# Optimization experiments

Measured on AMD Instinct MI355X. Metric: run time of the kernel, lower is better.

Reference implementation:

```python
import jax, jax.numpy as jnp
import numpy as np

B, T, D, H = 4, 2048, 1024, 16
HD = D // H  # head_dim = 64
SCALE = HD ** -0.5


def setup_inputs() -> dict:
    key = jax.random.key(0)
    k1, k2, k3 = jax.random.split(key, 3)
    x = jax.random.normal(k1, (B, T, D), dtype=jnp.float32)
    # xavier-uniform-like scaling for weights
    qkv_w = jax.random.normal(k2, (3 * D, D), dtype=jnp.float32) * (2.0 / (4 * D)) ** 0.5
    out_w = jax.random.normal(k3, (D, D), dtype=jnp.float32) * (1.0 / D) ** 0.5
    out_b = jnp.zeros((D,), dtype=jnp.float32)
    return {"x": x, "qkv_w": qkv_w, "out_w": out_w, "out_b": out_b}


def reference(x, qkv_w, out_w, out_b):
    Bx, Tx, _ = x.shape
    # qkv projection (nn.Linear: x @ W^T), no bias
    qkv = jnp.einsum('btd,ed->bte', x, qkv_w)  # [B,T,3D]
    qkv = qkv.reshape(Bx, Tx, 3, H, HD).transpose(2, 0, 3, 1, 4)  # [3,B,H,T,hd]
    q, k, v = qkv[0], qkv[1], qkv[2]
    scores = jnp.einsum('bhqd,bhkd->bhqk', q, k) * SCALE  # [B,H,T,T]
    causal = jnp.triu(jnp.ones((Tx, Tx), dtype=bool), k=1)
    scores = jnp.where(causal, -jnp.inf, scores)
    weights = jax.nn.softmax(scores, axis=-1)
    out = jnp.einsum('bhqk,bhkd->bhqd', weights, v)  # [B,H,T,hd]
    out = out.transpose(0, 2, 1, 3).reshape(Bx, Tx, D)
    return jnp.einsum('btd,ed->bte', out, out_w) + out_b
```

## Files before the change

kernel.cpp:

```cpp
#include <hip/hip_runtime.h>
#include <stdint.h>


typedef __bf16 bfx8 __attribute__((ext_vector_type(8)));
typedef float f32x4 __attribute__((ext_vector_type(4)));
typedef float f32x16 __attribute__((ext_vector_type(16)));

__device__ __forceinline__ uint16_t f2b(float f) {
  uint32_t u = __float_as_uint(f);
  u += 0x7fff + ((u >> 16) & 1);
  return (uint16_t)(u >> 16);
}

__device__ __forceinline__ uint32_t cvt_pk(float lo, float hi) {
  uint32_t r;
  asm("v_cvt_pk_bf16_f32 %0, %1, %2" : "=v"(r) : "v"(lo), "v"(hi));
  return r;
}

__device__ __forceinline__ void gld16(const void* g, void* l) {
  __builtin_amdgcn_global_load_lds((const __attribute__((address_space(1))) void*)g,
                                   (__attribute__((address_space(3))) void*)l,
                                   16, 0, 0);
}

__global__ __launch_bounds__(256) void cvt_all(const float* __restrict__ x,
                                               const float* __restrict__ w1,
                                               const float* __restrict__ w2,
                                               uint16_t* __restrict__ xb,
                                               uint16_t* __restrict__ w1b,
                                               uint16_t* __restrict__ w2b) {
  int i = blockIdx.x * 256 + threadIdx.x;
  const float* in;
  uint16_t* out;
  if (i < 1048576) { in = x; out = xb; }
  else if (i < 1048576 + 393216) { in = w1; out = w1b; i -= 1048576; }
  else { in = w2; out = w2b; i -= 1048576 + 393216; }
  float4 a = ((const float4*)in)[2 * i];
  float4 b = ((const float4*)in)[2 * i + 1];
  union { uint16_t u[8]; uint4 v; } pk;
  pk.u[0] = f2b(a.x); pk.u[1] = f2b(a.y); pk.u[2] = f2b(a.z); pk.u[3] = f2b(a.w);
  pk.u[4] = f2b(b.x); pk.u[5] = f2b(b.y); pk.u[6] = f2b(b.z); pk.u[7] = f2b(b.w);
  ((uint4*)out)[i] = pk.v;
}

template <int OUTF32>
__global__ __launch_bounds__(256) void gemm_bt(const uint16_t* __restrict__ A,
                                               const uint16_t* __restrict__ B,
                                               void* __restrict__ Cout,
                                               const float* __restrict__ bias,
                                               int M, int N, int K, int nbx, int nwg) {
  __shared__ alignas(16) uint16_t As[2][128 * 32];
  __shared__ alignas(16) uint16_t Bs[2][128 * 32];

  int did = blockIdx.x;
  int wg = (did & 7) * (nwg >> 3) + (did >> 3);
  int bx = wg % nbx, by = wg / nbx;
  int m0 = by * 128, n0 = bx * 128;

  int tid = threadIdx.x;
  int lane = tid & 63, wid = tid >> 6;
  int wm = wid >> 1, wn = wid & 1;

  int rs = wid * 16 + (lane >> 2);
  int cs = (lane & 3) * 8;

  f32x4 acc[4][4] = {};

  auto stage = [&](int buf, int kt) {
    int k0 = kt * 32;
    gld16(&A[(size_t)(m0 + rs) * K + k0 + cs],      &As[buf][wid * 512]);
    gld16(&A[(size_t)(m0 + rs + 64) * K + k0 + cs], &As[buf][wid * 512 + 2048]);
    gld16(&B[(size_t)(n0 + rs) * K + k0 + cs],      &Bs[buf][wid * 512]);
    gld16(&B[(size_t)(n0 + rs + 64) * K + k0 + cs], &Bs[buf][wid * 512 + 2048]);
  };

  stage(0, 0);
  __syncthreads();

  int nk = K >> 5;
  int cur = 0;
  int ko = (lane >> 4) * 8;
  for (int kt = 0; kt < nk; ++kt) {
    if (kt + 1 < nk) stage(cur ^ 1, kt + 1);
    bfx8 a[4], b[4];
#pragma unroll
    for (int mi = 0; mi < 4; ++mi)
      a[mi] = *(const bfx8*)&As[cur][(wm * 64 + mi * 16 + (lane & 15)) * 32 + ko];
#pragma unroll
    for (int ni = 0; ni < 4; ++ni)
      b[ni] = *(const bfx8*)&Bs[cur][(wn * 64 + ni * 16 + (lane & 15)) * 32 + ko];
#pragma unroll
    for (int mi = 0; mi < 4; ++mi)
#pragma unroll
      for (int ni = 0; ni < 4; ++ni)
        acc[mi][ni] =
            __builtin_amdgcn_mfma_f32_16x16x32_bf16(a[mi], b[ni], acc[mi][ni], 0, 0, 0);
    __syncthreads();
    cur ^= 1;
  }

#pragma unroll
  for (int mi = 0; mi < 4; ++mi) {
    int row = m0 + wm * 64 + mi * 16 + ((lane >> 4) << 2);
#pragma unroll
    for (int ni = 0; ni < 4; ++ni) {
      int col = n0 + wn * 64 + ni * 16 + (lane & 15);
#pragma unroll
      for (int r = 0; r < 4; ++r) {
        float v = acc[mi][ni][r];
        if (OUTF32)
          ((float*)Cout)[(size_t)(row + r) * N + col] = v + bias[col];
        else
          ((uint16_t*)Cout)[(size_t)(row + r) * N + col] = f2b(v);
      }
    }
  }
}

__global__ __launch_bounds__(256, 2) void flash_attn(const uint16_t* __restrict__ qkv,
                                                     uint16_t* __restrict__ attnb) {
  const int T = 2048, D3 = 3072;
  const float CSC = 0.125f * 1.44269504f;
  __shared__ alignas(16) uint16_t Ks[3][64 * 64];
  __shared__ alignas(16) uint16_t Vt[3][64 * 64];

  int did = blockIdx.x;
  int c = did & 255;
  int j = did >> 8;
  int bh = c >> 2, tr = c & 3;
  int b = bh >> 4, h = bh & 15;

  int tid = threadIdx.x, lane = tid & 63, wid = tid >> 6;
  int l31 = lane & 31, hi = lane >> 5;
  int swz = (lane & 7) << 3;

  size_t base = (size_t)b * T * D3;
  int hoff = h * 64;
  const uint16_t* kbase = &qkv[base + 1024 + hoff];
  const uint16_t* vbase = &qkv[base + 2048 + hoff];

  int krow = wid * 16 + (lane >> 3);
  int kc = ((lane & 7) << 3) ^ ((krow & 7) << 3);
  int vr = (tid & 31) * 2;
  int vc = (tid >> 5) * 8;

  int nparts = (j == 2) ? 2 : 1;
  for (int p = 0; p < nparts; ++p) {
    int qb = (j == 0) ? (15 - tr) : (j == 1) ? (8 + tr) : ((p == 0) ? (7 - tr) : tr);
    int q0 = qb << 7;
    int qw = q0 + wid * 32;
    int ntile = 2 * qb + 2;

    float mC = -1e30f, l_r = 0.f;
    f32x16 acc0 = {}, acc1 = {};
    bfx8 pf[4];
    int smax_prev = -1, vb_prev = 0;

    bfx8 qf[4];
    {
      const uint16_t* qp = &qkv[base + (size_t)(qw + l31) * D3 + hoff + 8 * hi];
#pragma unroll
      for (int h4 = 0; h4 < 4; ++h4) qf[h4] = *(const bfx8*)(qp + 16 * h4);
    }

    uint4 vA0, vA1, vB0, vB1;

    auto loadV = [&](int kv0, uint4& r0, uint4& r1) {
      r0 = *(const uint4*)&vbase[(size_t)(kv0 + vr) * D3 + vc];
      r1 = *(const uint4*)&vbase[(size_t)(kv0 + vr + 1) * D3 + vc];
    };
    auto stageK = [&](int buf, int kv0) {
      gld16(&kbase[(size_t)(kv0 + krow) * D3 + kc], &Ks[buf][wid * 1024]);
      gld16(&kbase[(size_t)(kv0 + krow + 8) * D3 + kc], &Ks[buf][wid * 1024 + 512]);
    };
    auto writeV = [&](int vb, const uint4& r0, const uint4& r1) {
      union { uint4 v; uint16_t u[8]; } x, y;
      x.v = r0; y.v = r1;
#pragma unroll
      for (int jj = 0; jj < 8; ++jj) {
        int hd = vc + jj;
        uint32_t pk = (uint32_t)x.u[jj] | ((uint32_t)y.u[jj] << 16);
        *(uint32_t*)&Vt[vb][hd * 64 + (vr ^ ((hd & 7) << 3))] = pk;
      }
    };
    auto doPV = [&]() {
      const uint16_t* vp = &Vt[vb_prev][0];
      __builtin_amdgcn_s_setprio(1);
#pragma unroll
      for (int s = 0; s < 4; ++s) {
        if (s <= smax_prev) {
          bfx8 v0 = *(const bfx8*)&vp[l31 * 64 + ((16 * s + 8 * hi) ^ swz)];
          acc0 = __builtin_amdgcn_mfma_f32_32x32x16_bf16(v0, pf[s], acc0, 0, 0, 0);
          bfx8 v1 = *(const bfx8*)&vp[(32 + l31) * 64 + ((16 * s + 8 * hi) ^ swz)];
          acc1 = __builtin_amdgcn_mfma_f32_32x32x16_bf16(v1, pf[s], acc1, 0, 0, 0);
        }
      }
      __builtin_amdgcn_s_setprio(0);
    };

    loadV(0, vA0, vA1);
    stageK(0, 0);
    writeV(0, vA0, vA1);
    loadV(64, vB0, vB1);
    stageK(1, 64);
    asm volatile("s_waitcnt vmcnt(0) lgkmcnt(0)" ::: "memory");
    __builtin_amdgcn_s_barrier();
    __builtin_amdgcn_sched_barrier(0);

    auto subiter = [&](int t, uint4& f0, uint4& f1, uint4& c0, uint4& c1) {
      int kv0 = t << 6;
      bool issue = (t + 2 < ntile);
      if (issue) {
        loadV((t + 2) << 6, f0, f1);
        stageK((t + 2) % 3, (t + 2) << 6);
      }
      bool active = (kv0 <= qw);
      int tmax = (qw > kv0) ? 2 : 1;
      f32x16 st0 = {}, st1 = {};
      if (active) {
        const uint16_t* kp = &Ks[t % 3][0];
        __builtin_amdgcn_s_setprio(1);
#pragma unroll
        for (int h4 = 0; h4 < 4; ++h4) {
          bfx8 kf0 = *(const bfx8*)&kp[l31 * 64 + ((16 * h4 + 8 * hi) ^ swz)];
          st0 = __builtin_amdgcn_mfma_f32_32x32x16_bf16(kf0, qf[h4], st0, 0, 0, 0);
          if (tmax == 2) {
            bfx8 kf1 = *(const bfx8*)&kp[(32 + l31) * 64 + ((16 * h4 + 8 * hi) ^ swz)];
            st1 = __builtin_amdgcn_mfma_f32_32x32x16_bf16(kf1, qf[h4], st1, 0, 0, 0);
          }
        }
        __builtin_amdgcn_s_setprio(0);
      }

      if (smax_prev >= 0) { doPV(); smax_prev = -1; }

      if (active) {
        int q = qw + l31;
        float mx0 = -1e30f, mx1 = -1e30f;
        if (kv0 == qw) {
#pragma unroll
          for (int r = 0; r < 16; ++r) {
            int kv = kv0 + (r & 3) + 8 * (r >> 2) + 4 * hi;
            float v = st0[r];
            if (kv > q) v = -1e30f;
            st0[r] = v;
            mx0 = fmaxf(mx0, v);
          }
        } else {
#pragma unroll
          for (int r = 0; r < 16; ++r) mx0 = fmaxf(mx0, st0[r]);
        }
        if (tmax == 2) {
          if (kv0 + 32 == qw) {
#pragma unroll
            for (int r = 0; r < 16; ++r) {
              int kv = kv0 + 32 + (r & 3) + 8 * (r >> 2) + 4 * hi;
              float v = st1[r];
              if (kv > q) v = -1e30f;
              st1[r] = v;
              mx1 = fmaxf(mx1, v);
            }
          } else {
#pragma unroll
            for (int r = 0; r < 16; ++r) mx1 = fmaxf(mx1, st1[r]);
          }
        }
        float mS = fmaxf(mx0, mx1) * CSC;
        if (!__all(mS - mC <= 8.0f)) {
          float mSp = fmaxf(mS, __shfl_xor(mS, 32));
          float mCn = fmaxf(mC, mSp);
          float fac = __builtin_amdgcn_exp2f(mC - mCn);
          mC = mCn;
          l_r *= fac;
          acc0 *= fac;
          acc1 *= fac;
        }
        float l0 = 0.f, l1 = 0.f, l2 = 0.f, l3 = 0.f;
#pragma unroll
        for (int r = 0; r < 16; r += 4) {
          float e0 = __builtin_amdgcn_exp2f(fmaf(st0[r], CSC, -mC));
          float e1 = __builtin_amdgcn_exp2f(fmaf(st0[r + 1], CSC, -mC));
          float e2 = __builtin_amdgcn_exp2f(fmaf(st0[r + 2], CSC, -mC));
          float e3 = __builtin_amdgcn_exp2f(fmaf(st0[r + 3], CSC, -mC));
          st0[r] = e0; st0[r + 1] = e1; st0[r + 2] = e2; st0[r + 3] = e3;
          l0 += e0; l1 += e1; l2 += e2; l3 += e3;
        }
        if (tmax == 2) {
#pragma unroll
          for (int r = 0; r < 16; r += 4) {
            float e0 = __builtin_amdgcn_exp2f(fmaf(st1[r], CSC, -mC));
            float e1 = __builtin_amdgcn_exp2f(fmaf(st1[r + 1], CSC, -mC));
            float e2 = __builtin_amdgcn_exp2f(fmaf(st1[r + 2], CSC, -mC));
            float e3 = __builtin_amdgcn_exp2f(fmaf(st1[r + 3], CSC, -mC));
            st1[r] = e0; st1[r + 1] = e1; st1[r + 2] = e2; st1[r + 3] = e3;
            l0 += e0; l1 += e1; l2 += e2; l3 += e3;
          }
        }
        l_r += (l0 + l1) + (l2 + l3);

        int smax = (qw + 31 - kv0) >> 4;
        if (smax > 3) smax = 3;
#pragma unroll
        for (int s = 0; s < 4; ++s) {
          if (s <= smax) {
            int pb = 8 * (s & 1);
            uint32_t W0, W1, W2, W3;
            if (s < 2) {
              W0 = cvt_pk(st0[pb + 0], st0[pb + 1]);
              W1 = cvt_pk(st0[pb + 2], st0[pb + 3]);
              W2 = cvt_pk(st0[pb + 4], st0[pb + 5]);
              W3 = cvt_pk(st0[pb + 6], st0[pb + 7]);
            } else {
              W0 = cvt_pk(st1[pb + 0], st1[pb + 1]);
              W1 = cvt_pk(st1[pb + 2], st1[pb + 3]);
              W2 = cvt_pk(st1[pb + 4], st1[pb + 5]);
              W3 = cvt_pk(st1[pb + 6], st1[pb + 7]);
            }
            auto rA = __builtin_amdgcn_permlane32_swap(W0, W2, false, false);
            auto rB = __builtin_amdgcn_permlane32_swap(W1, W3, false, false);
            union { uint32_t u[4]; bfx8 v; } pk;
            pk.u[0] = rA[0]; pk.u[1] = rB[0]; pk.u[2] = rA[1]; pk.u[3] = rB[1];
            pf[s] = pk.v;
          }
        }
        smax_prev = smax;
        vb_prev = t % 3;
      }

      if (t + 1 < ntile) writeV((t + 1) % 3, c0, c1);

      if (issue)
        asm volatile("s_waitcnt vmcnt(4) lgkmcnt(0)" ::: "memory");
      else
        asm volatile("s_waitcnt vmcnt(0) lgkmcnt(0)" ::: "memory");
      __builtin_amdgcn_s_barrier();
      __builtin_amdgcn_sched_barrier(0);
    };

    for (int t = 0; t < ntile; t += 2) {
      subiter(t, vA0, vA1, vB0, vB1);
      subiter(t + 1, vB0, vB1, vA0, vA1);
    }
    if (smax_prev >= 0) doPV();

    float l_tot = l_r + __shfl_xor(l_r, 32);
    __syncthreads();
    uint16_t* ow = ((uint16_t*)Ks) + wid * 2048;
    float rl = 1.0f / l_tot;
#pragma unroll
    for (int f = 0; f < 2; ++f) {
#pragma unroll
      for (int r = 0; r < 16; r += 2) {
        int hd = 32 * f + (r & 3) + 8 * (r >> 2) + 4 * hi;
        float v0 = (f ? acc1[r] : acc0[r]) * rl;
        float v1 = (f ? acc1[r + 1] : acc0[r + 1]) * rl;
        *(uint32_t*)&ow[l31 * 64 + (hd ^ ((l31 & 7) << 3))] = cvt_pk(v0, v1);
      }
    }
    int row = lane >> 1, cb = (lane & 1) * 32;
    int q = q0 + wid * 32 + row;
    int rs = (row & 7) << 3;
    uint16_t* dst = &attnb[(size_t)(b * T + q) * 1024 + hoff + cb];
#pragma unroll
    for (int cc = 0; cc < 4; ++cc)
      *(uint4*)&dst[cc * 8] = *(const uint4*)&ow[row * 64 + ((cb + cc * 8) ^ rs)];
    __syncthreads();
  }
}

extern "C" void kernel_launch(void* const* d_in, const int* in_sizes, int n_in,
                              void* d_out, int out_size, void* d_ws, size_t ws_size,
                              hipStream_t stream) {
  const float* x = (const float*)d_in[0];
  const float* qkv_w = (const float*)d_in[1];
  const float* out_w = (const float*)d_in[2];
  const float* out_b = (const float*)d_in[3];
  float* out = (float*)d_out;

  char* ws = (char*)d_ws;
  uint16_t* xb    = (uint16_t*)(ws);
  uint16_t* qkvb  = (uint16_t*)(ws + 16777216);
  uint16_t* attnb = (uint16_t*)(ws + 67108864);
  uint16_t* wqkvb = (uint16_t*)(ws + 83886080);
  uint16_t* wob   = (uint16_t*)(ws + 90177536);

  cvt_all<<<6144, 256, 0, stream>>>(x, qkv_w, out_w, xb, wqkvb, wob);

  gemm_bt<0><<<1536, 256, 0, stream>>>(xb, wqkvb, (void*)qkvb, nullptr,
                                       8192, 3072, 1024, 24, 1536);
  flash_attn<<<768, 256, 0, stream>>>(qkvb, attnb);
  gemm_bt<1><<<512, 256, 0, stream>>>(attnb, wob, (void*)out, out_b,
                                      8192, 1024, 1024, 8, 512);
}
```

Measured before the change: 205.6 us.

## Use 256x256 triple-buffered QKV GEMM and pair causal query blocks in attention

Adds a new 512-thread GEMM kernel with 256x256 output tiles and a three-stage LDS pipeline for the QKV projection. Larger tiles give more reuse per loaded byte and fewer workgroups. The attention launch now gives each workgroup a pair of query blocks (15-a and a), which balances causal work evenly over 512 blocks instead of the earlier 768-block mixed scheme. The risks are lower occupancy and higher register pressure from the 8x4 accumulator tile, and fewer blocks to spread across the CUs.

```diff
diff --git a/kernel.cpp b/kernel.cpp
--- a/kernel.cpp
+++ b/kernel.cpp
@@ -44,6 +44,90 @@
   ((uint4*)out)[i] = pk.v;
 }
 
+__global__ __launch_bounds__(512, 2) void gemm256(const uint16_t* __restrict__ A,
+                                                  const uint16_t* __restrict__ B,
+                                                  uint16_t* __restrict__ C,
+                                                  int M, int N, int K, int nbx, int nwg) {
+  __shared__ alignas(16) uint16_t As[3][256 * 32];
+  __shared__ alignas(16) uint16_t Bs[3][256 * 32];
+
+  int did = blockIdx.x;
+  int wg = (did & 7) * (nwg >> 3) + (did >> 3);
+  int bx = wg % nbx, by = wg / nbx;
+  int m0 = by * 256, n0 = bx * 256;
+
+  int tid = threadIdx.x;
+  int lane = tid & 63, wid = tid >> 6;
+  int wm = wid >> 2, wn = wid & 3;
+  int l15 = lane & 15;
+
+  int sr = lane >> 2;
+  int sc = ((lane & 3) * 8) ^ ((sr & 3) << 3);
+  int rdc = ((lane >> 4) * 8) ^ ((lane & 3) << 3);
+
+  f32x4 acc[8][4] = {};
+
+  auto stage = [&](int buf, int kt) {
+    int k0 = kt * 32;
+#pragma unroll
+    for (int i = 0; i < 2; ++i) {
+      int ch = wid * 2 + i;
+      int row = ch * 16 + sr;
+      gld16(&A[(size_t)(m0 + row) * K + k0 + sc], &As[buf][ch * 512]);
+      gld16(&B[(size_t)(n0 + row) * K + k0 + sc], &Bs[buf][ch * 512]);
+    }
+  };
+
+  stage(0, 0);
+  stage(1, 1);
+  asm volatile("s_waitcnt vmcnt(0) lgkmcnt(0)" ::: "memory");
+  __builtin_amdgcn_s_barrier();
+  __builtin_amdgcn_sched_barrier(0);
+
+  int nk = K >> 5;
+  for (int kt = 0; kt < nk; ++kt) {
+    bool issue = (kt + 2 < nk);
+    if (issue) stage((kt + 2) % 3, kt + 2);
+
+    const uint16_t* ap = &As[kt % 3][0];
+    const uint16_t* bp = &Bs[kt % 3][0];
+    bfx8 a[8], b[4];
+#pragma unroll
+    for (int mi = 0; mi < 8; ++mi)
+      a[mi] = *(const bfx8*)&ap[(wm * 128 + mi * 16 + l15) * 32 + rdc];
+#pragma unroll
+    for (int ni = 0; ni < 4; ++ni)
+      b[ni] = *(const bfx8*)&bp[(wn * 64 + ni * 16 + l15) * 32 + rdc];
+    __builtin_amdgcn_s_setprio(1);
+#pragma unroll
+    for (int mi = 0; mi < 8; ++mi)
+#pragma unroll
+      for (int ni = 0; ni < 4; ++ni)
+        acc[mi][ni] =
+            __builtin_amdgcn_mfma_f32_16x16x32_bf16(a[mi], b[ni], acc[mi][ni], 0, 0, 0);
+    __builtin_amdgcn_s_setprio(0);
+
+    if (issue)
+      asm volatile("s_waitcnt vmcnt(4) lgkmcnt(0)" ::: "memory");
+    else
+      asm volatile("s_waitcnt vmcnt(0) lgkmcnt(0)" ::: "memory");
+    __builtin_amdgcn_s_barrier();
+    __builtin_amdgcn_sched_barrier(0);
+  }
+
+#pragma unroll
+  for (int mi = 0; mi < 8; ++mi) {
+    int row = m0 + wm * 128 + mi * 16 + ((lane >> 4) << 2);
+#pragma unroll
+    for (int ni = 0; ni < 4; ++ni) {
+      int col = n0 + wn * 64 + ni * 16 + l15;
+#pragma unroll
+      for (int r = 0; r < 4; ++r)
+        C[(size_t)(row + r) * N + col] = f2b(acc[mi][ni][r]);
+    }
+  }
+}
+
 template <int OUTF32>
 __global__ __launch_bounds__(256) void gemm_bt(const uint16_t* __restrict__ A,
                                                const uint16_t* __restrict__ B,
@@ -125,10 +209,9 @@
   __shared__ alignas(16) uint16_t Ks[3][64 * 64];
   __shared__ alignas(16) uint16_t Vt[3][64 * 64];
 
-  int did = blockIdx.x;
-  int c = did & 255;
-  int j = did >> 8;
-  int bh = c >> 2, tr = c & 3;
+  int d = blockIdx.x;
+  int bh = d & 63;
+  int a = d >> 6;
   int b = bh >> 4, h = bh & 15;
 
   int tid = threadIdx.x, lane = tid & 63, wid = tid >> 6;
@@ -145,9 +228,8 @@
   int vr = (tid & 31) * 2;
   int vc = (tid >> 5) * 8;
 
-  int nparts = (j == 2) ? 2 : 1;
-  for (int p = 0; p < nparts; ++p) {
-    int qb = (j == 0) ? (15 - tr) : (j == 1) ? (8 + tr) : ((p == 0) ? (7 - tr) : tr);
+  for (int p = 0; p < 2; ++p) {
+    int qb = (p == 0) ? (15 - a) : a;
     int q0 = qb << 7;
     int qw = q0 + wid * 32;
     int ntile = 2 * qb + 2;
@@ -387,9 +469,8 @@
 
   cvt_all<<<6144, 256, 0, stream>>>(x, qkv_w, out_w, xb, wqkvb, wob);
 
-  gemm_bt<0><<<1536, 256, 0, stream>>>(xb, wqkvb, (void*)qkvb, nullptr,
-                                       8192, 3072, 1024, 24, 1536);
-  flash_attn<<<768, 256, 0, stream>>>(qkvb, attnb);
+  gemm256<<<384, 512, 0, stream>>>(xb, wqkvb, qkvb, 8192, 3072, 1024, 12, 384);
+  flash_attn<<<512, 256, 0, stream>>>(qkvb, attnb);
   gemm_bt<1><<<512, 256, 0, stream>>>(attnb, wob, (void*)out, out_b,
                                       8192, 1024, 1024, 8, 512);
 }
```

Result: no change. 206.6 us (+0.5%).
